# Performance work log

Measured on AMD Instinct MI355X. Metric: run time of the kernel, lower is better.

Reference implementation:

```python
import jax, jax.numpy as jnp
import numpy as np

B, C, D, H, W = 2, 64, 8, 24, 24  # hidden_dim = C; N = D*H*W = 4608 tokens


def setup_inputs() -> dict:
    key = jax.random.key(0)
    ks = jax.random.split(key, 8)
    s = 1.0 / np.sqrt(C)  # fan-in style init for 1x1 conv weights
    return {
        "x": jax.random.normal(ks[0], (B, C, D, H, W), dtype=jnp.float32),
        "h": jax.random.normal(ks[1], (B, C, D, H, W), dtype=jnp.float32),
        "Wq": jax.random.normal(ks[2], (C, C), dtype=jnp.float32) * s,
        "bq": jax.random.normal(ks[3], (C,), dtype=jnp.float32) * s,
        "Wk": jax.random.normal(ks[4], (C, C), dtype=jnp.float32) * s,
        "bk": jax.random.normal(ks[5], (C,), dtype=jnp.float32) * s,
        "Wv": jax.random.normal(ks[6], (C, C), dtype=jnp.float32) * s,
        "bv": jax.random.normal(ks[7], (C,), dtype=jnp.float32) * s,
    }


def reference(x, h, Wq, bq, Wk, bk, Wv, bv):
    # 1x1 Conv3d == per-token linear over channels
    def proj(inp, Wt, bt):
        f = inp.reshape(inp.shape[0], inp.shape[1], -1)  # [B, C, N]
        return jnp.einsum('oc,bcn->bon', Wt, f) + bt[None, :, None]

    q = proj(x, Wq, bq)  # [B, C, N]
    k = proj(h, Wk, bk)  # [B, C, N]
    v = proj(h, Wv, bv)  # [B, C, N]

    scale = 1.0 / np.sqrt(k.shape[1])  # k.size(1) ** 0.5 == sqrt(C)
    scores = jnp.einsum('bcm,bcn->bmn', q, k) * scale  # [B, N, N]
    attn = jax.nn.softmax(scores, axis=-1)
    out = jnp.einsum('bcn,bmn->bcm', v, attn)  # [B, C, N]
    return out.reshape(h.shape)
```

## Files before the change

kernel.cpp:

```cpp
#include <hip/hip_runtime.h>
#include <hip/hip_bf16.h>

#define C_DIM 64
#define N_TOK 4608
#define NBLK  72
#define B_SZ  2
#define M128BLKS 36
#define NSPLIT 3
#define NSEG  4
#define SEGLEN 384
#define NT    6
#define KTILES 288
#define VTILES 72
#define OSTR  68

typedef __bf16 bf16x8 __attribute__((ext_vector_type(8)));
typedef float  f32x4  __attribute__((ext_vector_type(4)));


__device__ __forceinline__ void gemm_tile(
    const __hip_bfloat16* wmat, const bf16x8 bin[2], const float* bias,
    int col, int quad, f32x4 acc[4])
{
    #pragma unroll
    for (int ot = 0; ot < 4; ot++) {
        f32x4 a = (f32x4){0.f, 0.f, 0.f, 0.f};
        #pragma unroll
        for (int kh = 0; kh < 2; kh++) {
            bf16x8 wf = *(const bf16x8*)(wmat + (ot * 16 + col) * 72 +
                                         kh * 32 + quad * 8);
            a = __builtin_amdgcn_mfma_f32_16x16x32_bf16(wf, bin[kh], a, 0, 0, 0);
        }
        float4 b4 = *(const float4*)(bias + ot * 16 + quad * 4);
        a[0] += b4.x; a[1] += b4.y; a[2] += b4.z; a[3] += b4.w;
        acc[ot] = a;
    }
}

__global__ __launch_bounds__(256) void proj_kernel(
    const float* __restrict__ x,  const float* __restrict__ h,
    const float* __restrict__ Wq, const float* __restrict__ bq,
    const float* __restrict__ Wk, const float* __restrict__ bk,
    const float* __restrict__ Wv, const float* __restrict__ bv,
    __hip_bfloat16* __restrict__ qS, __hip_bfloat16* __restrict__ kS,
    __hip_bfloat16* __restrict__ vS)
{
    __shared__ __hip_bfloat16 wl[3 * 64 * 72];
    __shared__ __hip_bfloat16 xt[64 * 72];
    __shared__ __hip_bfloat16 ht[64 * 72];
    __shared__ __hip_bfloat16 vl[64 * 72];

    const int b  = blockIdx.x / NBLK;
    const int n0 = (blockIdx.x % NBLK) * 64;
    const int t  = threadIdx.x;

    #pragma unroll
    for (int mat = 0; mat < 3; mat++) {
        const float* W = (mat == 0) ? Wq : ((mat == 1) ? Wk : Wv);
        __hip_bfloat16* wd = wl + mat * (64 * 72);
        #pragma unroll
        for (int i = 0; i < 4; i++) {
            const int ch = i * 256 + t;
            const int o = ch >> 4, c0 = (ch & 15) * 4;
            float4 w4 = *(const float4*)(W + ch * 4);
            union { __hip_bfloat16 e[4]; uint2 v; } pk;
            pk.e[0] = __float2bfloat16(w4.x); pk.e[1] = __float2bfloat16(w4.y);
            pk.e[2] = __float2bfloat16(w4.z); pk.e[3] = __float2bfloat16(w4.w);
            *(uint2*)(wd + o * 72 + c0) = pk.v;
        }
    }
    #pragma unroll
    for (int i = 0; i < 4; i++) {
        const int ch = i * 256 + t;
        const int c = ch >> 4, n4 = (ch & 15) * 4;
        float4 x4 = *(const float4*)(x + (size_t)(b * C_DIM + c) * N_TOK + n0 + n4);
        float4 h4 = *(const float4*)(h + (size_t)(b * C_DIM + c) * N_TOK + n0 + n4);
        xt[(n4 + 0) * 72 + c] = __float2bfloat16(x4.x);
        xt[(n4 + 1) * 72 + c] = __float2bfloat16(x4.y);
        xt[(n4 + 2) * 72 + c] = __float2bfloat16(x4.z);
        xt[(n4 + 3) * 72 + c] = __float2bfloat16(x4.w);
        ht[(n4 + 0) * 72 + c] = __float2bfloat16(h4.x);
        ht[(n4 + 1) * 72 + c] = __float2bfloat16(h4.y);
        ht[(n4 + 2) * 72 + c] = __float2bfloat16(h4.z);
        ht[(n4 + 3) * 72 + c] = __float2bfloat16(h4.w);
    }
    __syncthreads();

    const int wave = t >> 6, lane = t & 63;
    const int col = lane & 15, quad = lane >> 4;

    bf16x8 xb[2], hb[2];
    #pragma unroll
    for (int kh = 0; kh < 2; kh++) {
        xb[kh] = *(const bf16x8*)(xt + (wave * 16 + col) * 72 + kh * 32 + quad * 8);
        hb[kh] = *(const bf16x8*)(ht + (wave * 16 + col) * 72 + kh * 32 + quad * 8);
    }

    f32x4 acc[4];

    gemm_tile(wl + 0 * (64 * 72), xb, bq, col, quad, acc);
    {
        const size_t tile16 = (size_t)b * KTILES + (n0 >> 4) + wave;
        const float SC = 0.125f * 1.44269504088896f;
        #pragma unroll
        for (int ot = 0; ot < 4; ot++) {
            union { __hip_bfloat16 e[4]; uint2 v; } pk;
            #pragma unroll
            for (int r = 0; r < 4; r++) pk.e[r] = __float2bfloat16(acc[ot][r] * SC);
            *(uint2*)(qS + (tile16 << 10) + (ot >> 1) * 512 +
                      ((ot * 2 + (quad >> 1)) & 3) * 128 + col * 8 +
                      (quad & 1) * 4) = pk.v;
        }
    }

    gemm_tile(wl + 1 * (64 * 72), hb, bk, col, quad, acc);
    {
        const int t_l = (wave >> 1) * 2 + ((col >> 2) & 1);
        const int row = ((wave * 2 + (col >> 3)) & 3) * 4 + (col & 3);
        const size_t tile16 = (size_t)b * KTILES + (n0 >> 4) + t_l;
        #pragma unroll
        for (int ot = 0; ot < 4; ot++) {
            union { __hip_bfloat16 e[4]; uint2 v; } pk;
            #pragma unroll
            for (int r = 0; r < 4; r++) pk.e[r] = __float2bfloat16(acc[ot][r]);
            *(uint2*)(kS + (tile16 << 10) + (ot >> 1) * 512 +
                      ((ot * 2 + (quad >> 1)) & 3) * 128 + row * 8 +
                      (quad & 1) * 4) = pk.v;
        }
    }

    gemm_tile(wl + 2 * (64 * 72), hb, bv, col, quad, acc);
    #pragma unroll
    for (int ot = 0; ot < 4; ot++)
        #pragma unroll
        for (int r = 0; r < 4; r++)
            vl[(ot * 16 + quad * 4 + r) * 72 + wave * 16 + col] =
                __float2bfloat16(acc[ot][r]);
    __syncthreads();
    {
        const size_t vbase = ((size_t)(b * VTILES) + (n0 >> 6)) << 12;
        #pragma unroll
        for (int rep = 0; rep < 2; rep++) {
            const int ch = rep * 256 + t;
            const int cc = ch >> 7, hf = (ch >> 6) & 1;
            const int qd = (ch >> 4) & 3, c2 = ch & 15;
            *(uint4*)(vS + vbase + (size_t)ch * 8) =
                *(const uint4*)(vl + (cc * 16 + c2) * 72 + hf * 32 + qd * 8);
        }
    }
}

__global__ __launch_bounds__(512) void attn_kernel(
    const __hip_bfloat16* __restrict__ qS,
    const __hip_bfloat16* __restrict__ kS,
    const __hip_bfloat16* __restrict__ vS,
    float* __restrict__ Pb, float* __restrict__ Lb)
{
    __shared__ float o_lds[2][NSEG][16][OSTR];
    __shared__ float lstat[2][NSEG][64];

    const int idx  = blockIdx.x;
    const int b    = idx / (M128BLKS * NSPLIT);
    const int rem  = idx % (M128BLKS * NSPLIT);
    const int mblk = rem / NSPLIT;
    const int ns   = rem % NSPLIT;
    const int wave = threadIdx.x >> 6;
    const int lane = threadIdx.x & 63;
    const int col  = lane & 15;
    const int quad = lane >> 4;
    const int mg   = wave >> 2;
    const int seg  = wave & 3;
    const int m0   = mblk * 128 + mg * 64;

    float* Pns = Pb + (size_t)ns * (B_SZ * C_DIM * N_TOK);
    float* Lns = Lb + (size_t)ns * (B_SZ * N_TOK);

    const __hip_bfloat16* qp =
        qS + (((size_t)b * KTILES + (m0 >> 4)) << 10) + lane * 8;
    bf16x8 qa[4][2];
    #pragma unroll
    for (int ms = 0; ms < 4; ms++) {
        qa[ms][0] = *(const bf16x8*)(qp + ms * 1024);
        qa[ms][1] = *(const bf16x8*)(qp + ms * 1024 + 512);
    }

    f32x4 accO[4][4];
    #pragma unroll
    for (int ms = 0; ms < 4; ms++)
        #pragma unroll
        for (int cc = 0; cc < 4; cc++)
            accO[ms][cc] = (f32x4){0.f, 0.f, 0.f, 0.f};
    float rsum[4] = {0.f, 0.f, 0.f, 0.f};

    const int nbeg = ns * (NSEG * SEGLEN) + seg * SEGLEN;

    #pragma unroll 1
    for (int t = 0; t < NT; t++) {
        const int n0 = nbeg + t * 64;
        const __hip_bfloat16* kt =
            kS + (((size_t)b * KTILES + (n0 >> 4)) << 10) + lane * 8;
        bf16x8 ka[8];
        #pragma unroll
        for (int j = 0; j < 4; j++) {
            ka[2 * j]     = *(const bf16x8*)(kt + (j << 10));
            ka[2 * j + 1] = *(const bf16x8*)(kt + (j << 10) + 512);
        }
        const __hip_bfloat16* vt =
            vS + ((((size_t)b * VTILES) + (n0 >> 6)) << 12) + lane * 8;
        bf16x8 va[8];
        #pragma unroll
        for (int cc = 0; cc < 4; cc++) {
            va[2 * cc]     = *(const bf16x8*)(vt + cc * 1024);
            va[2 * cc + 1] = *(const bf16x8*)(vt + cc * 1024 + 512);
        }

        #pragma unroll
        for (int ms = 0; ms < 4; ms++) {
            f32x4 s[4];
            #pragma unroll
            for (int j = 0; j < 4; j++) {
                s[j] = __builtin_amdgcn_mfma_f32_16x16x32_bf16(
                           ka[2 * j], qa[ms][0],
                           (f32x4){0.f, 0.f, 0.f, 0.f}, 0, 0, 0);
                s[j] = __builtin_amdgcn_mfma_f32_16x16x32_bf16(
                           ka[2 * j + 1], qa[ms][1], s[j], 0, 0, 0);
            }
            union { __hip_bfloat16 e[8]; bf16x8 v; } p0, p1;
            float ps = 0.f;
            #pragma unroll
            for (int j = 0; j < 2; j++)
                #pragma unroll
                for (int r = 0; r < 4; r++) {
                    float e0 = __builtin_amdgcn_exp2f(s[j][r]);
                    float e1 = __builtin_amdgcn_exp2f(s[2 + j][r]);
                    ps += e0 + e1;
                    p0.e[j * 4 + r] = __float2bfloat16(e0);
                    p1.e[j * 4 + r] = __float2bfloat16(e1);
                }
            rsum[ms] += ps;
            #pragma unroll
            for (int cc = 0; cc < 4; cc++) {
                accO[ms][cc] = __builtin_amdgcn_mfma_f32_16x16x32_bf16(
                                   va[2 * cc], p0.v, accO[ms][cc], 0, 0, 0);
                accO[ms][cc] = __builtin_amdgcn_mfma_f32_16x16x32_bf16(
                                   va[2 * cc + 1], p1.v, accO[ms][cc], 0, 0, 0);
            }
        }
    }

    #pragma unroll
    for (int ms = 0; ms < 4; ms++) {
        rsum[ms] += __shfl_xor(rsum[ms], 16);
        rsum[ms] += __shfl_xor(rsum[ms], 32);
    }
    if (quad == 0) {
        #pragma unroll
        for (int ms = 0; ms < 4; ms++) lstat[mg][seg][ms * 16 + col] = rsum[ms];
    }

    #pragma unroll
    for (int p = 0; p < 4; p++) {
        #pragma unroll
        for (int cc = 0; cc < 4; cc++)
            *(f32x4*)(&o_lds[mg][seg][col][cc * 16 + quad * 4]) = accO[p][cc];
        __syncthreads();
        {
            const int t   = threadIdx.x;
            const int mgR = t >> 8;
            const int c   = (t >> 2) & 63;
            const int mq  = t & 3;
            f32x4 os = (f32x4){0.f, 0.f, 0.f, 0.f};
            f32x4 ls = (f32x4){0.f, 0.f, 0.f, 0.f};
            #pragma unroll
            for (int sgm = 0; sgm < NSEG; sgm++)
                #pragma unroll
                for (int j = 0; j < 4; j++) {
                    os[j] += o_lds[mgR][sgm][mq * 4 + j][c];
                    ls[j] += lstat[mgR][sgm][p * 16 + mq * 4 + j];
                }
            const int mabs = mblk * 128 + mgR * 64 + p * 16 + mq * 4;
            *(f32x4*)(Pns + ((size_t)b * C_DIM + c) * N_TOK + mabs) = os;
            if (c == 0)
                *(f32x4*)(Lns + (size_t)b * N_TOK + mabs) = ls;
        }
        __syncthreads();
    }
}

__global__ __launch_bounds__(256) void norm_kernel(
    const float* __restrict__ Pb, const float* __restrict__ Lb,
    float* __restrict__ out)
{
    const size_t stride = (size_t)B_SZ * C_DIM * N_TOK;
    const size_t f = ((size_t)blockIdx.x * 256 + threadIdx.x) * 4;
    f32x4 o = *(const f32x4*)(Pb + f) +
              *(const f32x4*)(Pb + stride + f) +
              *(const f32x4*)(Pb + 2 * stride + f);
    const int b = (int)(f / ((size_t)C_DIM * N_TOK));
    const int m = (int)(f % N_TOK);
    const size_t lf = (size_t)b * N_TOK + m;
    const size_t lstride = (size_t)B_SZ * N_TOK;
    f32x4 l = *(const f32x4*)(Lb + lf) +
              *(const f32x4*)(Lb + lstride + lf) +
              *(const f32x4*)(Lb + 2 * lstride + lf);
    f32x4 r;
    #pragma unroll
    for (int j = 0; j < 4; j++) r[j] = o[j] / l[j];
    *(f32x4*)(out + f) = r;
}

extern "C" void kernel_launch(void* const* d_in, const int* in_sizes, int n_in,
                              void* d_out, int out_size, void* d_ws, size_t ws_size,
                              hipStream_t stream) {
    const float* x  = (const float*)d_in[0];
    const float* h  = (const float*)d_in[1];
    const float* Wq = (const float*)d_in[2];
    const float* bq = (const float*)d_in[3];
    const float* Wk = (const float*)d_in[4];
    const float* bk = (const float*)d_in[5];
    const float* Wv = (const float*)d_in[6];
    const float* bv = (const float*)d_in[7];
    float* out = (float*)d_out;

    const size_t elems = (size_t)B_SZ * N_TOK * C_DIM;
    __hip_bfloat16* qS = (__hip_bfloat16*)d_ws;
    __hip_bfloat16* kS = qS + elems;
    __hip_bfloat16* vS = kS + elems;
    float* Pb = (float*)(vS + elems);
    float* Lb = Pb + NSPLIT * elems;

    proj_kernel<<<B_SZ * NBLK, 256, 0, stream>>>(x, h, Wq, bq, Wk, bk, Wv, bv,
                                                 qS, kS, vS);
    attn_kernel<<<B_SZ * M128BLKS * NSPLIT, 512, 0, stream>>>(qS, kS, vS, Pb, Lb);
    norm_kernel<<<576, 256, 0, stream>>>(Pb, Lb, out);
}
```

Measured before the change: 92.31 us.

## Fuse split-K normalization into attention kernel via last-block atomic counter

```diff
diff --git a/kernel.cpp b/kernel.cpp
--- a/kernel.cpp
+++ b/kernel.cpp
@@ -13,6 +13,8 @@
 #define KTILES 288
 #define VTILES 72
 #define OSTR  68
+#define PSTR  ((size_t)B_SZ * C_DIM * N_TOK)
+#define LSTR  ((size_t)B_SZ * N_TOK)
 
 typedef __bf16 bf16x8 __attribute__((ext_vector_type(8)));
 typedef float  f32x4  __attribute__((ext_vector_type(4)));
@@ -43,7 +45,7 @@
     const float* __restrict__ Wk, const float* __restrict__ bk,
     const float* __restrict__ Wv, const float* __restrict__ bv,
     __hip_bfloat16* __restrict__ qS, __hip_bfloat16* __restrict__ kS,
-    __hip_bfloat16* __restrict__ vS)
+    __hip_bfloat16* __restrict__ vS, int* __restrict__ cnt)
 {
     __shared__ __hip_bfloat16 wl[3 * 64 * 72];
     __shared__ __hip_bfloat16 xt[64 * 72];
@@ -51,8 +53,11 @@
     __shared__ __hip_bfloat16 vl[64 * 72];
 
     const int b  = blockIdx.x / NBLK;
-    const int n0 = (blockIdx.x % NBLK) * 64;
+    const int nb = blockIdx.x % NBLK;
+    const int n0 = nb * 64;
     const int t  = threadIdx.x;
+
+    if (nb < M128BLKS && t == 0) cnt[b * M128BLKS + nb] = 0;
 
     #pragma unroll
     for (int mat = 0; mat < 3; mat++) {
@@ -154,10 +159,12 @@
     const __hip_bfloat16* __restrict__ qS,
     const __hip_bfloat16* __restrict__ kS,
     const __hip_bfloat16* __restrict__ vS,
-    float* __restrict__ Pb, float* __restrict__ Lb)
+    float* __restrict__ Pb, float* __restrict__ Lb,
+    int* __restrict__ cnt, float* __restrict__ out)
 {
     __shared__ float o_lds[2][NSEG][16][OSTR];
     __shared__ float lstat[2][NSEG][64];
+    __shared__ int fin;
 
     const int idx  = blockIdx.x;
     const int b    = idx / (M128BLKS * NSPLIT);
@@ -172,8 +179,8 @@
     const int seg  = wave & 3;
     const int m0   = mblk * 128 + mg * 64;
 
-    float* Pns = Pb + (size_t)ns * (B_SZ * C_DIM * N_TOK);
-    float* Lns = Lb + (size_t)ns * (B_SZ * N_TOK);
+    float* Pns = Pb + (size_t)ns * PSTR;
+    float* Lns = Lb + (size_t)ns * LSTR;
 
     const __hip_bfloat16* qp =
         qS + (((size_t)b * KTILES + (m0 >> 4)) << 10) + lane * 8;
@@ -285,28 +292,36 @@
         }
         __syncthreads();
     }
-}
-
-__global__ __launch_bounds__(256) void norm_kernel(
-    const float* __restrict__ Pb, const float* __restrict__ Lb,
-    float* __restrict__ out)
-{
-    const size_t stride = (size_t)B_SZ * C_DIM * N_TOK;
-    const size_t f = ((size_t)blockIdx.x * 256 + threadIdx.x) * 4;
-    f32x4 o = *(const f32x4*)(Pb + f) +
-              *(const f32x4*)(Pb + stride + f) +
-              *(const f32x4*)(Pb + 2 * stride + f);
-    const int b = (int)(f / ((size_t)C_DIM * N_TOK));
-    const int m = (int)(f % N_TOK);
-    const size_t lf = (size_t)b * N_TOK + m;
-    const size_t lstride = (size_t)B_SZ * N_TOK;
-    f32x4 l = *(const f32x4*)(Lb + lf) +
-              *(const f32x4*)(Lb + lstride + lf) +
-              *(const f32x4*)(Lb + 2 * lstride + lf);
-    f32x4 r;
-    #pragma unroll
-    for (int j = 0; j < 4; j++) r[j] = o[j] / l[j];
-    *(f32x4*)(out + f) = r;
+
+    __threadfence();
+    __syncthreads();
+    if (threadIdx.x == 0) {
+        const int old = atomicAdd(&cnt[b * M128BLKS + mblk], 1);
+        fin = (old == NSPLIT - 1);
+    }
+    __syncthreads();
+    if (!fin) return;
+    __threadfence();
+
+    const int mbase = mblk * 128;
+    #pragma unroll
+    for (int i = 0; i < 4; i++) {
+        const int v  = i * 512 + (int)threadIdx.x;
+        const int c  = v >> 5;
+        const int mq = v & 31;
+        const size_t off = ((size_t)b * C_DIM + c) * N_TOK + mbase + mq * 4;
+        f32x4 o = *(const f32x4*)(Pb + off) +
+                  *(const f32x4*)(Pb + PSTR + off) +
+                  *(const f32x4*)(Pb + 2 * PSTR + off);
+        const size_t loff = (size_t)b * N_TOK + mbase + mq * 4;
+        f32x4 l = *(const f32x4*)(Lb + loff) +
+                  *(const f32x4*)(Lb + LSTR + loff) +
+                  *(const f32x4*)(Lb + 2 * LSTR + loff);
+        f32x4 r;
+        #pragma unroll
+        for (int j = 0; j < 4; j++) r[j] = o[j] / l[j];
+        *(f32x4*)(out + off) = r;
+    }
 }
 
 extern "C" void kernel_launch(void* const* d_in, const int* in_sizes, int n_in,
@@ -328,9 +343,10 @@
     __hip_bfloat16* vS = kS + elems;
     float* Pb = (float*)(vS + elems);
     float* Lb = Pb + NSPLIT * elems;
+    int*   cnt = (int*)(Lb + NSPLIT * (size_t)B_SZ * N_TOK);
 
     proj_kernel<<<B_SZ * NBLK, 256, 0, stream>>>(x, h, Wq, bq, Wk, bk, Wv, bv,
-                                                 qS, kS, vS);
-    attn_kernel<<<B_SZ * M128BLKS * NSPLIT, 512, 0, stream>>>(qS, kS, vS, Pb, Lb);
-    norm_kernel<<<576, 256, 0, stream>>>(Pb, Lb, out);
+                                                 qS, kS, vS, cnt);
+    attn_kernel<<<B_SZ * M128BLKS * NSPLIT, 512, 0, stream>>>(qS, kS, vS,
+                                                              Pb, Lb, cnt, out);
 }
```

New measurement: 143.6 us. 55.5% more time.
